# Performance work log

Measured on AMD Instinct MI355X. Metric: run time of the kernel, lower is better.

The kernel has to match this reference:

```python
import jax, jax.numpy as jnp
import numpy as np

DY = jnp.array([-1, -1, -1, 0, 0, 0, 1, 1, 1], dtype=jnp.float32)
DX = jnp.array([-1, 0, 1, -1, 0, 1, -1, 0, 1], dtype=jnp.float32)
REG = jnp.stack([DY, DX])  # (2,9) regular_matrix: row0 = dy, row1 = dx
EPS = 1e-5


def conv3x3(x, w, b):
    y = jax.lax.conv_general_dilated(x, w, (1, 1), ((1, 1), (1, 1)),
                                     dimension_numbers=('NCHW', 'OIHW', 'NCHW'))
    return y + b[None, :, None, None]


def batchnorm(x, gamma, beta):
    m = x.mean((0, 2, 3), keepdims=True)
    v = x.var((0, 2, 3), keepdims=True)
    return gamma[None, :, None, None] * (x - m) * jax.lax.rsqrt(v + EPS) + beta[None, :, None, None]


def make_offset(tm, tr):
    # tm: (N,4,H,W) per-pixel 2x2 matrix, tr: (N,2,H,W) translation
    N, _, H, W = tm.shape
    M = tm.transpose(0, 2, 3, 1).reshape(N, H, W, 2, 2)
    off = jnp.einsum('nhwij,jk->nhwik', M, REG) - REG          # (N,H,W,2,9)
    off = off.transpose(0, 4, 3, 1, 2)                          # (N,9,2,H,W)
    off = off + tr[:, None, :, :, :]                            # broadcast translation over K
    return off


def deform_conv(x, off, w):
    # x: (N,C,H,W), off: (N,9,2,H,W) with [...,0]=dy,[...,1]=dx, w: (Co,C,3,3)
    N, C, H, W = x.shape
    K = 9
    py = jnp.arange(H, dtype=x.dtype)[None, None, :, None] + DY[None, :, None, None] + off[:, :, 0]
    px = jnp.arange(W, dtype=x.dtype)[None, None, None, :] + DX[None, :, None, None] + off[:, :, 1]
    y0 = jnp.floor(py)
    x0 = jnp.floor(px)
    wy = py - y0
    wx = px - x0
    y0i = y0.astype(jnp.int32)
    x0i = x0.astype(jnp.int32)
    x_flat = x.reshape(N, C, H * W)

    def corner(yi, xi, wgt):
        valid = (yi >= 0) & (yi < H) & (xi >= 0) & (xi < W)
        idx = jnp.clip(yi, 0, H - 1) * W + jnp.clip(xi, 0, W - 1)   # (N,K,H,W)
        g = jax.vmap(lambda xf, ix: xf[:, ix])(x_flat, idx.reshape(N, -1))
        g = g.reshape(N, C, K, H, W)
        return g * (wgt * valid)[:, None]

    cols = (corner(y0i, x0i, (1 - wy) * (1 - wx))
            + corner(y0i, x0i + 1, (1 - wy) * wx)
            + corner(y0i + 1, x0i, wy * (1 - wx))
            + corner(y0i + 1, x0i + 1, wy * wx))
    Co = w.shape[0]
    return jnp.einsum('nckhw,ock->nohw', cols, w.reshape(Co, C, K))


def setup_inputs() -> dict:
    key = jax.random.key(0)
    ks = jax.random.split(key, 16)
    N, C, Co, H, W = 4, 256, 256, 64, 64
    s_off = 0.02   # small init so offsets stay near the regular grid
    s_w = 0.05
    return {
        'x': jax.random.normal(ks[0], (N, C, H, W), jnp.float32),
        'tm1_w': jax.random.normal(ks[1], (4, C, 3, 3), jnp.float32) * s_off,
        'tm1_b': jax.random.normal(ks[2], (4,), jnp.float32) * s_off,
        'tr1_w': jax.random.normal(ks[3], (2, C, 3, 3), jnp.float32) * s_off,
        'tr1_b': jax.random.normal(ks[4], (2,), jnp.float32) * s_off,
        'dcn1_w': jax.random.normal(ks[5], (Co, C, 3, 3), jnp.float32) * s_w,
        'bn1_g': jnp.ones((Co,), jnp.float32),
        'bn1_b': jnp.zeros((Co,), jnp.float32),
        'tm2_w': jax.random.normal(ks[6], (4, Co, 3, 3), jnp.float32) * s_off,
        'tm2_b': jax.random.normal(ks[7], (4,), jnp.float32) * s_off,
        'tr2_w': jax.random.normal(ks[8], (2, Co, 3, 3), jnp.float32) * s_off,
        'tr2_b': jax.random.normal(ks[9], (2,), jnp.float32) * s_off,
        'dcn2_w': jax.random.normal(ks[10], (Co, Co, 3, 3), jnp.float32) * s_w,
        'bn2_g': jnp.ones((Co,), jnp.float32),
        'bn2_b': jnp.zeros((Co,), jnp.float32),
    }


def reference(x, tm1_w, tm1_b, tr1_w, tr1_b, dcn1_w, bn1_g, bn1_b,
              tm2_w, tm2_b, tr2_w, tr2_b, dcn2_w, bn2_g, bn2_b):
    residual = x
    off1 = make_offset(conv3x3(x, tm1_w, tm1_b), conv3x3(x, tr1_w, tr1_b))
    out = deform_conv(x, off1, dcn1_w)
    out = jax.nn.relu(batchnorm(out, bn1_g, bn1_b))
    off2 = make_offset(conv3x3(out, tm2_w, tm2_b), conv3x3(out, tr2_w, tr2_b))
    out = deform_conv(out, off2, dcn2_w)
    out = batchnorm(out, bn2_g, bn2_b)
    return jax.nn.relu(out + residual)
```

## Files before the change

kernel.cpp:

```cpp
#include <hip/hip_runtime.h>
#include <hip/hip_bf16.h>

#define HH 64
#define WW 64
#define HWSZ 4096
#define NBATCH 4
#define CCH 256
#define NPIX 16384
#define CK 2304
#define EPSB 1e-5f

typedef __attribute__((ext_vector_type(8))) short bf16x8;
typedef __attribute__((ext_vector_type(4))) float f32x4;

static __device__ __forceinline__ unsigned short f2bf(float f){
  __hip_bfloat16 h = __float2bfloat16(f);
  return *(unsigned short*)&h;
}

#if __has_builtin(__builtin_amdgcn_global_load_lds)
#define GLD(S,D) __builtin_amdgcn_global_load_lds((const __attribute__((address_space(1))) void*)(S), \
                                                  (__attribute__((address_space(3))) void*)(D), 16, 0, 0)
#else
#define GLD(S,D) (*(bf16x8*)((char*)(D) + (threadIdx.x & 63)*16) = *(const bf16x8*)(S))
#endif

__global__ __launch_bounds__(256) void k_transpose_in(const float* __restrict__ x,
                                                      float* __restrict__ xT){
  __shared__ float tile[64][65];
  int hw0 = blockIdx.x * 64;
  int c0  = blockIdx.y * 64;
  int n   = blockIdx.z;
  int t = threadIdx.x;
  int col = t & 63, rb = t >> 6;
#pragma unroll
  for (int r = 0; r < 16; ++r){
    int cl = rb + r*4;
    tile[cl][col] = x[(size_t)(n*CCH + c0 + cl)*HWSZ + hw0 + col];
  }
  __syncthreads();
#pragma unroll
  for (int r = 0; r < 16; ++r){
    int hwl = rb + r*4;
    xT[(size_t)(n*HWSZ + hw0 + hwl)*CCH + c0 + col] = tile[col][hwl];
  }
}

__global__ void k_woff_perm(const float* __restrict__ tmw, const float* __restrict__ trw,
                            float* __restrict__ woff){
  int idx = blockIdx.x*256 + threadIdx.x;
  if (idx >= 9*6*CCH) return;
  int k = idx / (6*CCH); int rem = idx % (6*CCH); int j = rem >> 8; int c = rem & 255;
  float v = (j < 4) ? tmw[(size_t)(j*CCH + c)*9 + k]
                    : trw[(size_t)((j-4)*CCH + c)*9 + k];
  woff[idx] = v;
}

__global__ void k_wgemm_perm(const float* __restrict__ w, __hip_bfloat16* __restrict__ wp){
  int idx = blockIdx.x*256 + threadIdx.x;
  if (idx >= CCH*CK) return;
  int blk = idx >> 13;
  int e   = idx & 8191;
  int o   = e >> 5;
  int el  = e & 31;
  int tap = blk >> 3, cb = blk & 7;
  int c   = cb*32 + (el ^ (((o >> 1) & 3) << 3));
  wp[idx] = __float2bfloat16(w[(size_t)o*CK + c*9 + tap]);
}

__global__ __launch_bounds__(256) void k_offsets(const float* __restrict__ src,
    const float* __restrict__ wofft, const float* __restrict__ tmb,
    const float* __restrict__ trb, float* __restrict__ off){
  int t = threadIdx.x;
  int wid = t >> 6, lane = t & 63;
  int pbase = blockIdx.x*32 + wid*8;
  int n = pbase >> 12; int hw = pbase & 4095; int h = hw >> 6; int w0 = hw & 63;
  const float* base = src + (size_t)n*HWSZ*CCH + lane*4;

  float acc[8][6];
#pragma unroll
  for (int pi = 0; pi < 8; ++pi)
#pragma unroll
    for (int j = 0; j < 6; ++j) acc[pi][j] = 0.f;

  for (int k = 0; k < 9; ++k){
    int ky = k/3 - 1, kx = k%3 - 1;
    int yy = h + ky;
    if (yy < 0 || yy >= HH) continue;
    float4 wv[6];
#pragma unroll
    for (int j = 0; j < 6; ++j)
      wv[j] = *(const float4*)(wofft + ((k*6 + j) << 8) + lane*4);
#pragma unroll
    for (int pi = 0; pi < 8; ++pi){
      int xx = w0 + pi + kx;
      if (xx < 0 || xx >= WW) continue;
      float4 s4 = *(const float4*)(base + (size_t)(yy*WW + xx)*CCH);
#pragma unroll
      for (int j = 0; j < 6; ++j)
        acc[pi][j] += s4.x*wv[j].x + s4.y*wv[j].y + s4.z*wv[j].z + s4.w*wv[j].w;
    }
  }

#pragma unroll
  for (int pi = 0; pi < 8; ++pi)
#pragma unroll
    for (int j = 0; j < 6; ++j){
      float v = acc[pi][j];
#pragma unroll
      for (int m = 32; m >= 1; m >>= 1) v += __shfl_xor(v, m);
      acc[pi][j] = v;
    }

  float b0 = tmb[0], b1 = tmb[1], b2 = tmb[2], b3 = tmb[3];
  float c0 = trb[0], c1 = trb[1];
  if (lane < 18){
    int k = lane >> 1, comp = lane & 1;
    float dy = (float)(k/3 - 1), dx = (float)(k%3 - 1);
#pragma unroll
    for (int pi = 0; pi < 8; ++pi){
      int p = pbase + pi;
      float val;
      if (comp == 0)
        val = (acc[pi][0] + b0)*dy + (acc[pi][1] + b1)*dx - dy + acc[pi][4] + c0;
      else
        val = (acc[pi][2] + b2)*dy + (acc[pi][3] + b3)*dx - dx + acc[pi][5] + c1;
      off[((size_t)p*9 + k)*2 + comp] = val;
    }
  }
}

struct Gset { float4 a, b, c, d; };

__global__ __launch_bounds__(256) void k_dcn(const float* __restrict__ src,
    const float* __restrict__ off, const __hip_bfloat16* __restrict__ wp,
    float* __restrict__ gout){
  __shared__ __hip_bfloat16 Al[2*32*32];
  __shared__ __hip_bfloat16 Bl[4*256*32];
  __shared__ __align__(16) int   t_off[288][4];
  __shared__ __align__(16) float t_w[288][4];

  int t = threadIdx.x;
  int bid = blockIdx.x;
  int tile = (bid & 7)*64 + (bid >> 3);
  int pbase = tile * 32;

  for (int s = t; s < 288; s += 256){
    int px = s / 9, k = s - px*9;
    int p = pbase + px;
    int n = p >> 12; int hw = p & 4095; int h = hw >> 6; int w = hw & 63;
    float2 of = *(const float2*)(off + ((size_t)p*9 + k)*2);
    float py = (float)(h + k/3 - 1) + of.x;
    float px_ = (float)(w + (k - (k/3)*3) - 1) + of.y;
    float y0f = floorf(py), x0f = floorf(px_);
    float wy = py - y0f, wx = px_ - x0f;
    int y0 = (int)y0f, x0 = (int)x0f;
    int y1 = y0 + 1, x1 = x0 + 1;
    float w00 = (1.f-wy)*(1.f-wx), w01 = (1.f-wy)*wx;
    float w10 = wy*(1.f-wx),       w11 = wy*wx;
    if (y0 < 0 || y0 >= HH) { w00 = 0.f; w01 = 0.f; }
    if (y1 < 0 || y1 >= HH) { w10 = 0.f; w11 = 0.f; }
    if (x0 < 0 || x0 >= WW) { w00 = 0.f; w10 = 0.f; }
    if (x1 < 0 || x1 >= WW) { w01 = 0.f; w11 = 0.f; }
    int y0c = min(max(y0,0),HH-1), y1c = min(max(y1,0),HH-1);
    int x0c = min(max(x0,0),WW-1), x1c = min(max(x1,0),WW-1);
    int pbix = n << 12;
    t_off[s][0] = (pbix + y0c*WW + x0c) << 10;
    t_off[s][1] = (pbix + y0c*WW + x1c) << 10;
    t_off[s][2] = (pbix + y1c*WW + x0c) << 10;
    t_off[s][3] = (pbix + y1c*WW + x1c) << 10;
    t_w[s][0] = w00; t_w[s][1] = w01; t_w[s][2] = w10; t_w[s][3] = w11;
  }
  __syncthreads();

  int wid = t >> 6, lane = t & 63;
  int pxl = t >> 3, q = t & 7;
  const char* sbase = (const char*)src;
  const char* wpb = (const char*)wp;

  int abyte = pxl*64 + (((q >> 1) ^ ((pxl >> 1) & 3)) << 4) + (q & 1)*8;

  int kq = lane >> 4, fr = lane & 15;
  int abr0, abr1, bbr0, bbr1, bbr2, bbr3;
  {
    int a0 = 0*16 + fr;  abr0 = a0*64 + ((kq ^ ((a0 >> 1) & 3)) << 4);
    int a1 = 1*16 + fr;  abr1 = a1*64 + ((kq ^ ((a1 >> 1) & 3)) << 4);
    int o0 = wid*64 + 0*16 + fr;  bbr0 = o0*64 + ((kq ^ ((o0 >> 1) & 3)) << 4);
    int o1 = wid*64 + 1*16 + fr;  bbr1 = o1*64 + ((kq ^ ((o1 >> 1) & 3)) << 4);
    int o2 = wid*64 + 2*16 + fr;  bbr2 = o2*64 + ((kq ^ ((o2 >> 1) & 3)) << 4);
    int o3 = wid*64 + 3*16 + fr;  bbr3 = o3*64 + ((kq ^ ((o3 >> 1) & 3)) << 4);
  }

  f32x4 acc[2][4];
#pragma unroll
  for (int i = 0; i < 2; ++i)
#pragma unroll
    for (int j = 0; j < 4; ++j)
      acc[i][j] = (f32x4){0.f,0.f,0.f,0.f};

  Gset gA, gB;

  auto issue_gather = [&](int ktn, Gset& g){
    int slot = pxl*9 + (ktn >> 3);
    int chb = ((ktn & 7) << 7) + (q << 4);
    int4 o4 = *(const int4*)t_off[slot];
    g.a = *(const float4*)(sbase + (size_t)(unsigned)(o4.x + chb));
    g.b = *(const float4*)(sbase + (size_t)(unsigned)(o4.y + chb));
    g.c = *(const float4*)(sbase + (size_t)(unsigned)(o4.z + chb));
    g.d = *(const float4*)(sbase + (size_t)(unsigned)(o4.w + chb));
  };
  auto convert_write = [&](int ktc, Gset& g){
    int slot = pxl*9 + (ktc >> 3);
    float4 wv = *(const float4*)t_w[slot];
    float v0 = wv.x*g.a.x + wv.y*g.b.x + wv.z*g.c.x + wv.w*g.d.x;
    float v1 = wv.x*g.a.y + wv.y*g.b.y + wv.z*g.c.y + wv.w*g.d.y;
    float v2 = wv.x*g.a.z + wv.y*g.b.z + wv.z*g.c.z + wv.w*g.d.z;
    float v3 = wv.x*g.a.w + wv.y*g.b.w + wv.z*g.c.w + wv.w*g.d.w;
    ushort4 st; st.x = f2bf(v0); st.y = f2bf(v1); st.z = f2bf(v2); st.w = f2bf(v3);
    *(ushort4*)((char*)Al + (ktc & 1)*2048 + abyte) = st;
  };
  auto issue_B = [&](int ktb){
    const char* bsrc = wpb + (size_t)ktb*16384 + t*16;
    char* bdst = (char*)Bl + (ktb & 3)*16384 + wid*1024;
    GLD(bsrc,                bdst);
    GLD(bsrc + 4096,         bdst + 4096);
    GLD(bsrc + 8192,         bdst + 8192);
    GLD(bsrc + 12288,        bdst + 12288);
  };

  issue_B(0);
  issue_B(1);
  asm volatile("" ::: "memory");
  issue_gather(0, gA);
  issue_gather(1, gB);
  convert_write(0, gA);
  asm volatile("s_waitcnt lgkmcnt(0)" ::: "memory");
  __builtin_amdgcn_sched_barrier(0);
  __builtin_amdgcn_s_barrier();
  __builtin_amdgcn_sched_barrier(0);

  auto body = [&](int kt, Gset& gIss, Gset& gCnv){
    const char* Ac = (const char*)Al + (kt & 1)*2048;
    const char* Bc = (const char*)Bl + (kt & 3)*16384;
    bf16x8 av0 = *(const bf16x8*)(Ac + abr0);
    bf16x8 av1 = *(const bf16x8*)(Ac + abr1);
    bf16x8 bv0 = *(const bf16x8*)(Bc + bbr0);
    bf16x8 bv1 = *(const bf16x8*)(Bc + bbr1);
    bf16x8 bv2 = *(const bf16x8*)(Bc + bbr2);
    bf16x8 bv3 = *(const bf16x8*)(Bc + bbr3);
    if (kt <= 69) issue_B(kt + 2);
    asm volatile("" ::: "memory");
    if (kt <= 69) issue_gather(kt + 2, gIss);
    acc[0][0] = __builtin_amdgcn_mfma_f32_16x16x32_bf16(av0, bv0, acc[0][0], 0, 0, 0);
    acc[0][1] = __builtin_amdgcn_mfma_f32_16x16x32_bf16(av0, bv1, acc[0][1], 0, 0, 0);
    acc[0][2] = __builtin_amdgcn_mfma_f32_16x16x32_bf16(av0, bv2, acc[0][2], 0, 0, 0);
    acc[0][3] = __builtin_amdgcn_mfma_f32_16x16x32_bf16(av0, bv3, acc[0][3], 0, 0, 0);
    acc[1][0] = __builtin_amdgcn_mfma_f32_16x16x32_bf16(av1, bv0, acc[1][0], 0, 0, 0);
    acc[1][1] = __builtin_amdgcn_mfma_f32_16x16x32_bf16(av1, bv1, acc[1][1], 0, 0, 0);
    acc[1][2] = __builtin_amdgcn_mfma_f32_16x16x32_bf16(av1, bv2, acc[1][2], 0, 0, 0);
    acc[1][3] = __builtin_amdgcn_mfma_f32_16x16x32_bf16(av1, bv3, acc[1][3], 0, 0, 0);
    if (kt <= 70) convert_write(kt + 1, gCnv);
    asm volatile("s_waitcnt lgkmcnt(0)" ::: "memory");
    __builtin_amdgcn_sched_barrier(0);
    __builtin_amdgcn_s_barrier();
    __builtin_amdgcn_sched_barrier(0);
  };

  for (int kk = 0; kk < 72; kk += 2){
    body(kk + 0, gA, gB);
    body(kk + 1, gB, gA);
  }

#pragma unroll
  for (int mi = 0; mi < 2; ++mi)
#pragma unroll
    for (int ni = 0; ni < 4; ++ni){
      int rr = pbase + mi*16 + (lane>>4)*4;
      int cc = wid*64 + ni*16 + fr;
#pragma unroll
      for (int r = 0; r < 4; ++r)
        gout[(size_t)(rr + r)*CCH + cc] = acc[mi][ni][r];
    }
}

__global__ __launch_bounds__(256) void k_bn_stats(const float* __restrict__ v,
                                                  float* __restrict__ stats){
  int t = threadIdx.x;
  int p0 = blockIdx.x * 128;
  float s = 0.f, ss = 0.f;
  for (int i = 0; i < 128; ++i){
    float x = v[(size_t)(p0 + i)*CCH + t];
    s += x; ss += x*x;
  }
  atomicAdd(&stats[t], s);
  atomicAdd(&stats[CCH + t], ss);
}

__global__ __launch_bounds__(256) void k_bn_apply(const float* __restrict__ v,
    const float* __restrict__ stats, const float* __restrict__ g,
    const float* __restrict__ bb, float* __restrict__ y){
  const float inv = 1.f/16384.f;
  for (size_t i = (size_t)blockIdx.x*256 + threadIdx.x; i < (size_t)NPIX*CCH;
       i += (size_t)gridDim.x*256){
    int c = (int)(i & 255);
    float mean = stats[c]*inv;
    float var  = stats[CCH + c]*inv - mean*mean;
    float sc = g[c]*rsqrtf(var + EPSB);
    float sh = bb[c] - mean*sc;
    float val = fmaf(v[i], sc, sh);
    y[i] = val > 0.f ? val : 0.f;
  }
}

__global__ __launch_bounds__(256) void k_final(const float* __restrict__ v,
    const float* __restrict__ stats, const float* __restrict__ g,
    const float* __restrict__ bb, const float* __restrict__ x,
    float* __restrict__ out){
  __shared__ float tile[64][65];
  int hw0 = blockIdx.x * 64;
  int o0  = blockIdx.y * 64;
  int n   = blockIdx.z;
  int t = threadIdx.x;
  int col = t & 63, rb = t >> 6;
  const float inv = 1.f/16384.f;
#pragma unroll
  for (int r = 0; r < 16; ++r){
    int pl = rb + r*4;
    tile[pl][col] = v[(size_t)(n*HWSZ + hw0 + pl)*CCH + o0 + col];
  }
  __syncthreads();
#pragma unroll
  for (int r = 0; r < 16; ++r){
    int ol = rb + r*4;
    int o = o0 + ol;
    float mean = stats[o]*inv;
    float var  = stats[CCH + o]*inv - mean*mean;
    float sc = g[o]*rsqrtf(var + EPSB);
    float sh = bb[o] - mean*sc;
    size_t gi = (size_t)(n*CCH + o)*HWSZ + hw0 + col;
    float val = fmaf(tile[col][ol], sc, sh) + x[gi];
    out[gi] = val > 0.f ? val : 0.f;
  }
}

extern "C" void kernel_launch(void* const* d_in, const int* in_sizes, int n_in,
                              void* d_out, int out_size, void* d_ws, size_t ws_size,
                              hipStream_t stream){
  const float* x     = (const float*)d_in[0];
  const float* tm1_w = (const float*)d_in[1];
  const float* tm1_b = (const float*)d_in[2];
  const float* tr1_w = (const float*)d_in[3];
  const float* tr1_b = (const float*)d_in[4];
  const float* dcn1_w= (const float*)d_in[5];
  const float* bn1_g = (const float*)d_in[6];
  const float* bn1_b = (const float*)d_in[7];
  const float* tm2_w = (const float*)d_in[8];
  const float* tm2_b = (const float*)d_in[9];
  const float* tr2_w = (const float*)d_in[10];
  const float* tr2_b = (const float*)d_in[11];
  const float* dcn2_w= (const float*)d_in[12];
  const float* bn2_g = (const float*)d_in[13];
  const float* bn2_b = (const float*)d_in[14];
  float* out = (float*)d_out;

  char* ws = (char*)d_ws;
  size_t cursor = 0;
  auto alloc = [&](size_t bytes)->char*{
    char* p = ws + cursor; cursor += (bytes + 255) & ~(size_t)255; return p;
  };
  float* xT    = (float*)alloc((size_t)NPIX*CCH*4);
  float* ybuf  = (float*)alloc((size_t)NPIX*CCH*4);
  float* gout  = (float*)alloc((size_t)NPIX*CCH*4);
  float* offb  = (float*)alloc((size_t)NPIX*9*2*4);
  float* woff1 = (float*)alloc(9*6*CCH*4);
  float* woff2 = (float*)alloc(9*6*CCH*4);
  __hip_bfloat16* wg1 = (__hip_bfloat16*)alloc((size_t)CCH*CK*2);
  __hip_bfloat16* wg2 = (__hip_bfloat16*)alloc((size_t)CCH*CK*2);
  float* stats = (float*)alloc(1024*4);

  hipMemsetAsync(stats, 0, 1024*4, stream);
  k_transpose_in<<<dim3(64,4,4),256,0,stream>>>(x, xT);
  k_woff_perm<<<54,256,0,stream>>>(tm1_w, tr1_w, woff1);
  k_woff_perm<<<54,256,0,stream>>>(tm2_w, tr2_w, woff2);
  k_wgemm_perm<<<2304,256,0,stream>>>(dcn1_w, wg1);
  k_wgemm_perm<<<2304,256,0,stream>>>(dcn2_w, wg2);

  k_offsets<<<512,256,0,stream>>>(xT, woff1, tm1_b, tr1_b, offb);
  k_dcn<<<512,256,0,stream>>>(xT, offb, wg1, gout);
  k_bn_stats<<<128,256,0,stream>>>(gout, stats);
  k_bn_apply<<<2048,256,0,stream>>>(gout, stats, bn1_g, bn1_b, ybuf);

  k_offsets<<<512,256,0,stream>>>(ybuf, woff2, tm2_b, tr2_b, offb);
  k_dcn<<<512,256,0,stream>>>(ybuf, offb, wg2, gout);
  k_bn_stats<<<128,256,0,stream>>>(gout, stats + 512);
  k_final<<<dim3(64,4,4),256,0,stream>>>(gout, stats + 512, bn2_g, bn2_b, x, out);
}
```

Baseline: 201.9 us.

## Fuse BN statistics into deform-conv epilogue and shrink B buffer ring

```diff
diff --git a/kernel.cpp b/kernel.cpp
--- a/kernel.cpp
+++ b/kernel.cpp
@@ -134,9 +134,9 @@
 
 __global__ __launch_bounds__(256) void k_dcn(const float* __restrict__ src,
     const float* __restrict__ off, const __hip_bfloat16* __restrict__ wp,
-    float* __restrict__ gout){
+    float* __restrict__ gout, float* __restrict__ pbstats){
   __shared__ __hip_bfloat16 Al[2*32*32];
-  __shared__ __hip_bfloat16 Bl[4*256*32];
+  __shared__ __hip_bfloat16 Bl[2*256*32];
   __shared__ __align__(16) int   t_off[288][4];
   __shared__ __align__(16) float t_w[288][4];
 
@@ -221,7 +221,7 @@
   };
   auto issue_B = [&](int ktb){
     const char* bsrc = wpb + (size_t)ktb*16384 + t*16;
-    char* bdst = (char*)Bl + (ktb & 3)*16384 + wid*1024;
+    char* bdst = (char*)Bl + (ktb & 1)*16384 + wid*1024;
     GLD(bsrc,                bdst);
     GLD(bsrc + 4096,         bdst + 4096);
     GLD(bsrc + 8192,         bdst + 8192);
@@ -229,26 +229,22 @@
   };
 
   issue_B(0);
-  issue_B(1);
   asm volatile("" ::: "memory");
   issue_gather(0, gA);
   issue_gather(1, gB);
   convert_write(0, gA);
-  asm volatile("s_waitcnt lgkmcnt(0)" ::: "memory");
-  __builtin_amdgcn_sched_barrier(0);
-  __builtin_amdgcn_s_barrier();
-  __builtin_amdgcn_sched_barrier(0);
+  __syncthreads();
 
   auto body = [&](int kt, Gset& gIss, Gset& gCnv){
     const char* Ac = (const char*)Al + (kt & 1)*2048;
-    const char* Bc = (const char*)Bl + (kt & 3)*16384;
+    const char* Bc = (const char*)Bl + (kt & 1)*16384;
     bf16x8 av0 = *(const bf16x8*)(Ac + abr0);
     bf16x8 av1 = *(const bf16x8*)(Ac + abr1);
     bf16x8 bv0 = *(const bf16x8*)(Bc + bbr0);
     bf16x8 bv1 = *(const bf16x8*)(Bc + bbr1);
     bf16x8 bv2 = *(const bf16x8*)(Bc + bbr2);
     bf16x8 bv3 = *(const bf16x8*)(Bc + bbr3);
-    if (kt <= 69) issue_B(kt + 2);
+    if (kt <= 70) issue_B(kt + 1);
     asm volatile("" ::: "memory");
     if (kt <= 69) issue_gather(kt + 2, gIss);
     acc[0][0] = __builtin_amdgcn_mfma_f32_16x16x32_bf16(av0, bv0, acc[0][0], 0, 0, 0);
@@ -260,10 +256,7 @@
     acc[1][2] = __builtin_amdgcn_mfma_f32_16x16x32_bf16(av1, bv2, acc[1][2], 0, 0, 0);
     acc[1][3] = __builtin_amdgcn_mfma_f32_16x16x32_bf16(av1, bv3, acc[1][3], 0, 0, 0);
     if (kt <= 70) convert_write(kt + 1, gCnv);
-    asm volatile("s_waitcnt lgkmcnt(0)" ::: "memory");
-    __builtin_amdgcn_sched_barrier(0);
-    __builtin_amdgcn_s_barrier();
-    __builtin_amdgcn_sched_barrier(0);
+    __syncthreads();
   };
 
   for (int kk = 0; kk < 72; kk += 2){
@@ -275,25 +268,41 @@
   for (int mi = 0; mi < 2; ++mi)
 #pragma unroll
     for (int ni = 0; ni < 4; ++ni){
-      int rr = pbase + mi*16 + (lane>>4)*4;
+      int rr = pbase + mi*16 + kq*4;
       int cc = wid*64 + ni*16 + fr;
 #pragma unroll
       for (int r = 0; r < 4; ++r)
         gout[(size_t)(rr + r)*CCH + cc] = acc[mi][ni][r];
     }
-}
-
-__global__ __launch_bounds__(256) void k_bn_stats(const float* __restrict__ v,
-                                                  float* __restrict__ stats){
+  float* pbs = pbstats + (size_t)bid*512;
+#pragma unroll
+  for (int ni = 0; ni < 4; ++ni){
+    float s = 0.f, ss = 0.f;
+#pragma unroll
+    for (int mi = 0; mi < 2; ++mi)
+#pragma unroll
+      for (int r = 0; r < 4; ++r){
+        float v = acc[mi][ni][r];
+        s += v; ss += v*v;
+      }
+    s  += __shfl_xor(s, 16);  s  += __shfl_xor(s, 32);
+    ss += __shfl_xor(ss, 16); ss += __shfl_xor(ss, 32);
+    if (kq == 0){
+      int cc = wid*64 + ni*16 + fr;
+      pbs[cc]       = s;
+      pbs[256 + cc] = ss;
+    }
+  }
+}
+
+__global__ __launch_bounds__(256) void k_stats_reduce(const float* __restrict__ pb,
+                                                      float* __restrict__ so){
   int t = threadIdx.x;
-  int p0 = blockIdx.x * 128;
-  float s = 0.f, ss = 0.f;
-  for (int i = 0; i < 128; ++i){
-    float x = v[(size_t)(p0 + i)*CCH + t];
-    s += x; ss += x*x;
-  }
-  atomicAdd(&stats[t], s);
-  atomicAdd(&stats[CCH + t], ss);
+  int ofs = blockIdx.x * 256;
+  float s = 0.f;
+  for (int b = 0; b < 512; ++b)
+    s += pb[(size_t)b*512 + ofs + t];
+  so[ofs + t] = s;
 }
 
 __global__ __launch_bounds__(256) void k_bn_apply(const float* __restrict__ v,
@@ -377,8 +386,8 @@
   __hip_bfloat16* wg1 = (__hip_bfloat16*)alloc((size_t)CCH*CK*2);
   __hip_bfloat16* wg2 = (__hip_bfloat16*)alloc((size_t)CCH*CK*2);
   float* stats = (float*)alloc(1024*4);
-
-  hipMemsetAsync(stats, 0, 1024*4, stream);
+  float* pbstats = (float*)alloc((size_t)512*512*4);
+
   k_transpose_in<<<dim3(64,4,4),256,0,stream>>>(x, xT);
   k_woff_perm<<<54,256,0,stream>>>(tm1_w, tr1_w, woff1);
   k_woff_perm<<<54,256,0,stream>>>(tm2_w, tr2_w, woff2);
@@ -386,12 +395,12 @@
   k_wgemm_perm<<<2304,256,0,stream>>>(dcn2_w, wg2);
 
   k_offsets<<<512,256,0,stream>>>(xT, woff1, tm1_b, tr1_b, offb);
-  k_dcn<<<512,256,0,stream>>>(xT, offb, wg1, gout);
-  k_bn_stats<<<128,256,0,stream>>>(gout, stats);
+  k_dcn<<<512,256,0,stream>>>(xT, offb, wg1, gout, pbstats);
+  k_stats_reduce<<<2,256,0,stream>>>(pbstats, stats);
   k_bn_apply<<<2048,256,0,stream>>>(gout, stats, bn1_g, bn1_b, ybuf);
 
   k_offsets<<<512,256,0,stream>>>(ybuf, woff2, tm2_b, tr2_b, offb);
-  k_dcn<<<512,256,0,stream>>>(ybuf, offb, wg2, gout);
-  k_bn_stats<<<128,256,0,stream>>>(gout, stats + 512);
+  k_dcn<<<512,256,0,stream>>>(ybuf, offb, wg2, gout, pbstats);
+  k_stats_reduce<<<2,256,0,stream>>>(pbstats, stats + 512);
   k_final<<<dim3(64,4,4),256,0,stream>>>(gout, stats + 512, bn2_g, bn2_b, x, out);
 }
```

Measured after the change: 225.4 us. 11.6% more time.
